# Optimization experiments

Measured on AMD Instinct MI355X. Metric: run time of the kernel, lower is better.

Reference implementation:

```python
import jax, jax.numpy as jnp
import numpy as np

QMIN_A, QMAX_A = -128, 127  # int8 activation range
GROUPSIZE = 32


def per_token_quant_dequant(x):
    """Dynamic per-token asymmetric int8 fake-quant (torchao per_token_dynamic_quant)."""
    min_val = jnp.minimum(jnp.min(x, axis=-1, keepdims=True), 0.0)
    max_val = jnp.maximum(jnp.max(x, axis=-1, keepdims=True), 0.0)
    scale = (max_val - min_val) / float(QMAX_A - QMIN_A)
    scale = jnp.maximum(scale, jnp.finfo(x.dtype).eps)
    zp = jnp.clip(QMIN_A - jnp.round(min_val / scale), QMIN_A, QMAX_A)
    q = jnp.clip(jnp.round(x / scale) + zp, QMIN_A, QMAX_A)
    return (q - zp) * scale


def dequant_int4_grouped(w_int, w_scales, w_zeros):
    """w_int: [O, I] int4 values in [-8, 7]; scales/zeros: [O, I//GROUPSIZE]."""
    O, I = w_int.shape
    G = I // GROUPSIZE
    wg = w_int.reshape(O, G, GROUPSIZE).astype(w_scales.dtype)
    w_dq = (wg - w_zeros[:, :, None]) * w_scales[:, :, None]
    return w_dq.reshape(O, I)


def setup_inputs() -> dict:
    key = jax.random.key(0)
    k1, k2, k3 = jax.random.split(key, 3)
    B, S, D_IN, D_OUT = 4, 2048, 2048, 2048
    G = D_IN // GROUPSIZE
    x = jax.random.normal(k1, (B, S, D_IN), dtype=jnp.float32)
    w_int = jax.random.randint(k2, (D_OUT, D_IN), -8, 8, dtype=jnp.int32)
    w_scales = jax.random.uniform(k3, (D_OUT, G), dtype=jnp.float32) * 0.01 + 1e-3
    w_zeros = jnp.zeros((D_OUT, G), dtype=jnp.float32)
    return {"x": x, "w_int": w_int, "w_scales": w_scales, "w_zeros": w_zeros}


def reference(x, w_int, w_scales, w_zeros):
    x_dq = per_token_quant_dequant(x)                  # [B, S, I]
    w_dq = dequant_int4_grouped(w_int, w_scales, w_zeros)  # [O, I]
    return jnp.einsum("bsi,oi->bso", x_dq, w_dq)       # [B, S, O]
```

## Files before the change

### kernel.cpp

```cpp
#include <hip/hip_runtime.h>

#define M_DIM 8192
#define N_DIM 2048
#define K_DIM 2048

#define BM 256
#define BN 128
#define BK 64

#define AS1 __attribute__((address_space(1)))
#define AS3 __attribute__((address_space(3)))

typedef float f32x4 __attribute__((ext_vector_type(4)));
typedef short s16x8 __attribute__((ext_vector_type(8)));

__device__ __forceinline__ unsigned short f2bf(float f) {
  unsigned int u = __float_as_uint(f);
  u += 0x7FFFu + ((u >> 16) & 1u);
  return (unsigned short)(u >> 16);
}

__global__ __launch_bounds__(256) void quant_x_kernel(
    const float* __restrict__ x, unsigned short* __restrict__ A) {
  const int t   = blockIdx.x;
  const int tid = threadIdx.x;
  const float4* r4 = (const float4*)(x + (size_t)t * K_DIM);
  float4 v0 = r4[tid];
  float4 v1 = r4[tid + 256];

  float mn = fminf(fminf(fminf(v0.x, v0.y), fminf(v0.z, v0.w)),
                   fminf(fminf(v1.x, v1.y), fminf(v1.z, v1.w)));
  float mx = fmaxf(fmaxf(fmaxf(v0.x, v0.y), fmaxf(v0.z, v0.w)),
                   fmaxf(fmaxf(v1.x, v1.y), fmaxf(v1.z, v1.w)));
#pragma unroll
  for (int off = 32; off > 0; off >>= 1) {
    mn = fminf(mn, __shfl_xor(mn, off));
    mx = fmaxf(mx, __shfl_xor(mx, off));
  }
  __shared__ float smn[4], smx[4];
  if ((tid & 63) == 0) { smn[tid >> 6] = mn; smx[tid >> 6] = mx; }
  __syncthreads();
  mn = fminf(fminf(smn[0], smn[1]), fminf(smn[2], smn[3]));
  mx = fmaxf(fmaxf(smx[0], smx[1]), fmaxf(smx[2], smx[3]));
  mn = fminf(mn, 0.0f);
  mx = fmaxf(mx, 0.0f);

  float scale = (mx - mn) / 255.0f;
  scale = fmaxf(scale, 1.1920928955078125e-07f);
  const float inv = 1.0f / scale;
  float zp = -128.0f - rintf(mn * inv);
  zp = fminf(fmaxf(zp, -128.0f), 127.0f);

  ushort4* Ao = (ushort4*)(A + (size_t)t * K_DIM);
  {
    float q; ushort4 r;
    q = rintf(v0.x * inv) + zp; q = fminf(fmaxf(q, -128.f), 127.f); r.x = f2bf((q - zp) * scale);
    q = rintf(v0.y * inv) + zp; q = fminf(fmaxf(q, -128.f), 127.f); r.y = f2bf((q - zp) * scale);
    q = rintf(v0.z * inv) + zp; q = fminf(fmaxf(q, -128.f), 127.f); r.z = f2bf((q - zp) * scale);
    q = rintf(v0.w * inv) + zp; q = fminf(fmaxf(q, -128.f), 127.f); r.w = f2bf((q - zp) * scale);
    Ao[tid] = r;
  }
  {
    float q; ushort4 r;
    q = rintf(v1.x * inv) + zp; q = fminf(fmaxf(q, -128.f), 127.f); r.x = f2bf((q - zp) * scale);
    q = rintf(v1.y * inv) + zp; q = fminf(fmaxf(q, -128.f), 127.f); r.y = f2bf((q - zp) * scale);
    q = rintf(v1.z * inv) + zp; q = fminf(fmaxf(q, -128.f), 127.f); r.z = f2bf((q - zp) * scale);
    q = rintf(v1.w * inv) + zp; q = fminf(fmaxf(q, -128.f), 127.f); r.w = f2bf((q - zp) * scale);
    Ao[tid + 256] = r;
  }
}

__global__ __launch_bounds__(256) void prep_w_kernel(
    const int* __restrict__ w, const float* __restrict__ ws,
    const float* __restrict__ wz, unsigned short* __restrict__ W) {
  const int idx = blockIdx.x * 256 + threadIdx.x;
  const int o  = idx >> 8;
  const int ii = (idx & 255) * 8;
  const int g  = ii >> 5;
  const float s = ws[o * 64 + g];
  const float z = wz[o * 64 + g];
  const int4* wp = (const int4*)(w + (size_t)o * K_DIM + ii);
  int4 a = wp[0], b = wp[1];
  ushort4 r0, r1;
  r0.x = f2bf(((float)a.x - z) * s);
  r0.y = f2bf(((float)a.y - z) * s);
  r0.z = f2bf(((float)a.z - z) * s);
  r0.w = f2bf(((float)a.w - z) * s);
  r1.x = f2bf(((float)b.x - z) * s);
  r1.y = f2bf(((float)b.y - z) * s);
  r1.z = f2bf(((float)b.z - z) * s);
  r1.w = f2bf(((float)b.w - z) * s);
  ushort4* Wo = (ushort4*)(W + (size_t)o * K_DIM + ii);
  Wo[0] = r0;
  Wo[1] = r1;
}

__global__ __launch_bounds__(256, 2) void gemm_kernel(
    const unsigned short* __restrict__ A,
    const unsigned short* __restrict__ B,
    float* __restrict__ C) {
  __shared__ unsigned short As[2 * BM * BK];
  __shared__ unsigned short Bs[BN * BK];

  const int tid  = threadIdx.x;
  const int id  = blockIdx.y * 16 + blockIdx.x;
  const int nid = (id & 7) * 64 + (id >> 3);
  const int bm  = (nid >> 4) * BM;
  const int bn  = (nid & 15) * BN;

  const int lane = tid & 63;
  const int wv   = tid >> 6;
  const int waveM = (wv >> 1) * 128;
  const int waveN = (wv & 1) * 64;
  const int quad = lane >> 4;
  const int l16  = lane & 15;

  const int trow = tid >> 3;
  const int phys = (tid & 7) ^ (trow & 7);
  const unsigned short* ag = A + (size_t)(bm + trow) * K_DIM + phys * 8;

  const unsigned short* bgp = B + (size_t)(bn + trow) * K_DIM + (tid & 7) * 8;
  int bwoff[4];
#pragma unroll
  for (int j = 0; j < 4; ++j) {
    const int row = trow + j * 32;
    bwoff[j] = row * BK + (((tid & 7) ^ (row & 7)) * 8);
  }

  int aoff[8], boff[4];
#pragma unroll
  for (int mi = 0; mi < 8; ++mi)
    aoff[mi] = (waveM + mi * 16 + l16) * BK + ((quad ^ (l16 & 7)) * 8);
#pragma unroll
  for (int ni = 0; ni < 4; ++ni)
    boff[ni] = (waveN + ni * 16 + l16) * BK + ((quad ^ (l16 & 7)) * 8);

  f32x4 acc[8][4] = {};
  s16x8 breg[4];

#pragma unroll
  for (int j = 0; j < 8; ++j)
    __builtin_amdgcn_global_load_lds((const AS1 void*)(ag + (size_t)j * 32 * K_DIM),
                                     (AS3 void*)(&As[tid * 8 + j * 2048]), 16, 0, 0);
#pragma unroll
  for (int j = 0; j < 4; ++j)
    breg[j] = *(const s16x8*)(bgp + (size_t)j * 32 * K_DIM);
#pragma unroll
  for (int j = 0; j < 4; ++j)
    *(s16x8*)&Bs[bwoff[j]] = breg[j];
  __syncthreads();

  for (int k0 = 0; k0 < K_DIM; k0 += BK) {
    const int p  = (k0 >> 6) & 1;
    const int kn = k0 + BK;
    if (kn < K_DIM) {
#pragma unroll
      for (int j = 0; j < 8; ++j)
        __builtin_amdgcn_global_load_lds(
            (const AS1 void*)(ag + (size_t)j * 32 * K_DIM + kn),
            (AS3 void*)(&As[((p ^ 1) << 14) + tid * 8 + j * 2048]), 16, 0, 0);
#pragma unroll
      for (int j = 0; j < 4; ++j)
        breg[j] = *(const s16x8*)(bgp + (size_t)j * 32 * K_DIM + kn);
    }

#pragma unroll
    for (int kk = 0; kk < 2; ++kk) {
      s16x8 af[8], bf[4];
#pragma unroll
      for (int mi = 0; mi < 8; ++mi)
        af[mi] = *(const s16x8*)&As[(p << 14) + (aoff[mi] ^ (kk * 32))];
#pragma unroll
      for (int ni = 0; ni < 4; ++ni)
        bf[ni] = *(const s16x8*)&Bs[boff[ni] ^ (kk * 32)];
#pragma unroll
      for (int mi = 0; mi < 8; ++mi)
#pragma unroll
        for (int ni = 0; ni < 4; ++ni)
          acc[mi][ni] = __builtin_amdgcn_mfma_f32_16x16x32_bf16(
              af[mi], bf[ni], acc[mi][ni], 0, 0, 0);
    }
    __syncthreads();
    if (kn < K_DIM) {
#pragma unroll
      for (int j = 0; j < 4; ++j)
        *(s16x8*)&Bs[bwoff[j]] = breg[j];
    }
    __syncthreads();
  }

#pragma unroll
  for (int mi = 0; mi < 8; ++mi) {
#pragma unroll
    for (int ni = 0; ni < 4; ++ni) {
      const int o = bn + waveN + ni * 16 + l16;
#pragma unroll
      for (int r = 0; r < 4; ++r) {
        const int t = bm + waveM + mi * 16 + quad * 4 + r;
        C[(size_t)t * N_DIM + o] = acc[mi][ni][r];
      }
    }
  }
}

extern "C" void kernel_launch(void* const* d_in, const int* in_sizes, int n_in,
                              void* d_out, int out_size, void* d_ws, size_t ws_size,
                              hipStream_t stream) {
  const float* x        = (const float*)d_in[0];
  const int*   w_int    = (const int*)d_in[1];
  const float* w_scales = (const float*)d_in[2];
  const float* w_zeros  = (const float*)d_in[3];
  float* out = (float*)d_out;

  unsigned short* Aq = (unsigned short*)d_ws;
  unsigned short* Wq = Aq + (size_t)M_DIM * K_DIM;

  quant_x_kernel<<<M_DIM, 256, 0, stream>>>(x, Aq);
  prep_w_kernel<<<(N_DIM * (K_DIM / 8)) / 256, 256, 0, stream>>>(w_int, w_scales, w_zeros, Wq);
  dim3 grid(N_DIM / BN, M_DIM / BM);
  gemm_kernel<<<grid, 256, 0, stream>>>(Aq, Wq, out);
}
```

Baseline: 195.4 us.

## Enlarge GEMM tile to 256x256 with 8 waves and phased LDS pipeline

The GEMM block tile grows from 256x128 to 256x256 and runs 512 threads (8 waves). B is now double-buffered and loaded straight into LDS with global_load_lds, replacing the register round-trip. The K loop is split into four phases separated by explicit barriers. Each phase interleaves LDS fragment reads, async prefetch of the next tile and an MFMA quad under raised priority, to hide memory latency and cut the number of global reads per FLOP. The cost is 128 KB of LDS per block, which limits occupancy, plus more barriers per iteration; the launch_bounds of 2 blocks per CU may not be reachable.

```diff
diff --git a/kernel.cpp b/kernel.cpp
--- a/kernel.cpp
+++ b/kernel.cpp
@@ -5,8 +5,9 @@
 #define K_DIM 2048
 
 #define BM 256
-#define BN 128
+#define BN 256
 #define BK 64
+#define NT (K_DIM / BK)
 
 #define AS1 __attribute__((address_space(1)))
 #define AS3 __attribute__((address_space(3)))
@@ -95,37 +96,92 @@
   Wo[1] = r1;
 }
 
-__global__ __launch_bounds__(256, 2) void gemm_kernel(
+
+#define PHASE_BAR()                                  \
+  do {                                               \
+    __builtin_amdgcn_sched_barrier(0);               \
+    __builtin_amdgcn_s_barrier();                    \
+    __builtin_amdgcn_sched_barrier(0);               \
+  } while (0)
+
+#define READ_AF(MH)                                                         \
+  do {                                                                      \
+    _Pragma("unroll") for (int i = 0; i < 4; ++i) {                         \
+      _Pragma("unroll") for (int kk = 0; kk < 2; ++kk) {                    \
+        af[i][kk] = *(const s16x8*)&Ab[aoff[(MH) * 4 + i] ^ (kk * 32)];     \
+      }                                                                     \
+    }                                                                       \
+  } while (0)
+
+#define READ_BF(NH)                                                         \
+  do {                                                                      \
+    _Pragma("unroll") for (int j = 0; j < 2; ++j) {                         \
+      _Pragma("unroll") for (int kk = 0; kk < 2; ++kk) {                    \
+        bf[NH][j][kk] = *(const s16x8*)&Bb[boff[(NH) * 2 + j] ^ (kk * 32)]; \
+      }                                                                     \
+    }                                                                       \
+  } while (0)
+
+#define MFMA_QUAD(MH, NH)                                                   \
+  do {                                                                      \
+    __builtin_amdgcn_s_setprio(1);                                          \
+    _Pragma("unroll") for (int kk = 0; kk < 2; ++kk) {                      \
+      _Pragma("unroll") for (int i = 0; i < 4; ++i) {                       \
+        _Pragma("unroll") for (int j = 0; j < 2; ++j) {                     \
+          acc[(MH) * 4 + i][(NH) * 2 + j] =                                 \
+              __builtin_amdgcn_mfma_f32_16x16x32_bf16(                      \
+                  af[i][kk], bf[NH][j][kk],                                 \
+                  acc[(MH) * 4 + i][(NH) * 2 + j], 0, 0, 0);                \
+        }                                                                   \
+      }                                                                     \
+    }                                                                       \
+    __builtin_amdgcn_s_setprio(0);                                          \
+  } while (0)
+
+#define STAGE_A(KN, DSTP)                                                   \
+  do {                                                                      \
+    _Pragma("unroll") for (int j = 0; j < 4; ++j) {                         \
+      __builtin_amdgcn_global_load_lds(                                     \
+          (const AS1 void*)(ag + (size_t)j * 64 * K_DIM + (KN)),            \
+          (AS3 void*)(&As[(DSTP) * (BM * BK) + tid * 8 + j * 4096]),        \
+          16, 0, 0);                                                        \
+    }                                                                       \
+  } while (0)
+
+#define STAGE_B(KN, DSTP)                                                   \
+  do {                                                                      \
+    _Pragma("unroll") for (int j = 0; j < 4; ++j) {                         \
+      __builtin_amdgcn_global_load_lds(                                     \
+          (const AS1 void*)(bg + (size_t)j * 64 * K_DIM + (KN)),            \
+          (AS3 void*)(&Bs[(DSTP) * (BN * BK) + tid * 8 + j * 4096]),        \
+          16, 0, 0);                                                        \
+    }                                                                       \
+  } while (0)
+
+__global__ __launch_bounds__(512, 2) void gemm_kernel(
     const unsigned short* __restrict__ A,
     const unsigned short* __restrict__ B,
     float* __restrict__ C) {
   __shared__ unsigned short As[2 * BM * BK];
-  __shared__ unsigned short Bs[BN * BK];
-
-  const int tid  = threadIdx.x;
-  const int id  = blockIdx.y * 16 + blockIdx.x;
-  const int nid = (id & 7) * 64 + (id >> 3);
-  const int bm  = (nid >> 4) * BM;
-  const int bn  = (nid & 15) * BN;
-
-  const int lane = tid & 63;
-  const int wv   = tid >> 6;
-  const int waveM = (wv >> 1) * 128;
-  const int waveN = (wv & 1) * 64;
-  const int quad = lane >> 4;
-  const int l16  = lane & 15;
+  __shared__ unsigned short Bs[2 * BN * BK];
+
+  const int tid = threadIdx.x;
+  const int id  = blockIdx.y * 8 + blockIdx.x;
+  const int nid = (id & 7) * 32 + (id >> 3);
+  const int bm  = (nid >> 3) * BM;
+  const int bn  = (nid & 7) * BN;
+
+  const int lane  = tid & 63;
+  const int wv    = tid >> 6;
+  const int waveM = (wv >> 2) * 128;
+  const int waveN = (wv & 3) * 64;
+  const int quad  = lane >> 4;
+  const int l16   = lane & 15;
 
   const int trow = tid >> 3;
   const int phys = (tid & 7) ^ (trow & 7);
   const unsigned short* ag = A + (size_t)(bm + trow) * K_DIM + phys * 8;
-
-  const unsigned short* bgp = B + (size_t)(bn + trow) * K_DIM + (tid & 7) * 8;
-  int bwoff[4];
-#pragma unroll
-  for (int j = 0; j < 4; ++j) {
-    const int row = trow + j * 32;
-    bwoff[j] = row * BK + (((tid & 7) ^ (row & 7)) * 8);
-  }
+  const unsigned short* bg = B + (size_t)(bn + trow) * K_DIM + phys * 8;
 
   int aoff[8], boff[4];
 #pragma unroll
@@ -136,57 +192,46 @@
     boff[ni] = (waveN + ni * 16 + l16) * BK + ((quad ^ (l16 & 7)) * 8);
 
   f32x4 acc[8][4] = {};
-  s16x8 breg[4];
-
-#pragma unroll
-  for (int j = 0; j < 8; ++j)
-    __builtin_amdgcn_global_load_lds((const AS1 void*)(ag + (size_t)j * 32 * K_DIM),
-                                     (AS3 void*)(&As[tid * 8 + j * 2048]), 16, 0, 0);
-#pragma unroll
-  for (int j = 0; j < 4; ++j)
-    breg[j] = *(const s16x8*)(bgp + (size_t)j * 32 * K_DIM);
-#pragma unroll
-  for (int j = 0; j < 4; ++j)
-    *(s16x8*)&Bs[bwoff[j]] = breg[j];
-  __syncthreads();
-
-  for (int k0 = 0; k0 < K_DIM; k0 += BK) {
-    const int p  = (k0 >> 6) & 1;
-    const int kn = k0 + BK;
-    if (kn < K_DIM) {
-#pragma unroll
-      for (int j = 0; j < 8; ++j)
-        __builtin_amdgcn_global_load_lds(
-            (const AS1 void*)(ag + (size_t)j * 32 * K_DIM + kn),
-            (AS3 void*)(&As[((p ^ 1) << 14) + tid * 8 + j * 2048]), 16, 0, 0);
-#pragma unroll
-      for (int j = 0; j < 4; ++j)
-        breg[j] = *(const s16x8*)(bgp + (size_t)j * 32 * K_DIM + kn);
-    }
-
-#pragma unroll
-    for (int kk = 0; kk < 2; ++kk) {
-      s16x8 af[8], bf[4];
-#pragma unroll
-      for (int mi = 0; mi < 8; ++mi)
-        af[mi] = *(const s16x8*)&As[(p << 14) + (aoff[mi] ^ (kk * 32))];
-#pragma unroll
-      for (int ni = 0; ni < 4; ++ni)
-        bf[ni] = *(const s16x8*)&Bs[boff[ni] ^ (kk * 32)];
-#pragma unroll
-      for (int mi = 0; mi < 8; ++mi)
-#pragma unroll
-        for (int ni = 0; ni < 4; ++ni)
-          acc[mi][ni] = __builtin_amdgcn_mfma_f32_16x16x32_bf16(
-              af[mi], bf[ni], acc[mi][ni], 0, 0, 0);
-    }
-    __syncthreads();
-    if (kn < K_DIM) {
-#pragma unroll
-      for (int j = 0; j < 4; ++j)
-        *(s16x8*)&Bs[bwoff[j]] = breg[j];
-    }
-    __syncthreads();
+
+  STAGE_A(0, 0);
+  STAGE_B(0, 0);
+  __builtin_amdgcn_sched_barrier(0);
+  asm volatile("s_waitcnt vmcnt(0)" ::: "memory");
+  __builtin_amdgcn_s_barrier();
+  __builtin_amdgcn_sched_barrier(0);
+
+  for (int t = 0; t < NT; ++t) {
+    const int p = t & 1;
+    const unsigned short* Ab = &As[p * (BM * BK)];
+    const unsigned short* Bb = &Bs[p * (BN * BK)];
+    const int kn = (t + 1) * BK;
+    const bool pref = (t + 1) < NT;
+
+    s16x8 af[4][2];
+    s16x8 bf[2][2][2];
+
+    READ_AF(0);
+    READ_BF(0);
+    if (pref) STAGE_A(kn, p ^ 1);
+    PHASE_BAR();
+    MFMA_QUAD(0, 0);
+    PHASE_BAR();
+
+    READ_BF(1);
+    if (pref) STAGE_B(kn, p ^ 1);
+    PHASE_BAR();
+    MFMA_QUAD(0, 1);
+    PHASE_BAR();
+
+    READ_AF(1);
+    PHASE_BAR();
+    MFMA_QUAD(1, 1);
+    PHASE_BAR();
+
+    MFMA_QUAD(1, 0);
+    __builtin_amdgcn_sched_barrier(0);
+    asm volatile("s_waitcnt vmcnt(0)" ::: "memory");
+    PHASE_BAR();
   }
 
 #pragma unroll
@@ -196,8 +241,8 @@
       const int o = bn + waveN + ni * 16 + l16;
 #pragma unroll
       for (int r = 0; r < 4; ++r) {
-        const int t = bm + waveM + mi * 16 + quad * 4 + r;
-        C[(size_t)t * N_DIM + o] = acc[mi][ni][r];
+        const int row = bm + waveM + mi * 16 + quad * 4 + r;
+        C[(size_t)row * N_DIM + o] = acc[mi][ni][r];
       }
     }
   }
@@ -218,5 +263,5 @@
   quant_x_kernel<<<M_DIM, 256, 0, stream>>>(x, Aq);
   prep_w_kernel<<<(N_DIM * (K_DIM / 8)) / 256, 256, 0, stream>>>(w_int, w_scales, w_zeros, Wq);
   dim3 grid(N_DIM / BN, M_DIM / BM);
-  gemm_kernel<<<grid, 256, 0, stream>>>(Aq, Wq, out);
-}
+  gemm_kernel<<<grid, 512, 0, stream>>>(Aq, Wq, out);
+}
```

Measured after the change: 192.3 us. No clear change (-1.6%).
